# Performance work log

Hardware: AMD Instinct MI355X
Metric: run time of the kernel (lower is better)

## Reference

```python
import jax, jax.numpy as jnp
import numpy as np

B, T, F, H, FC1, NC = 16384, 56, 56, 20, 128, 2


def setup_inputs() -> dict:
    key = jax.random.key(0)
    ks = jax.random.split(key, 12)
    s_in = 1.0 / np.sqrt(H)  # PyTorch GRU init scale
    d = {
        'x': jax.random.normal(ks[0], (B, T, F), jnp.float32),
        'W_ih0': jax.random.uniform(ks[1], (3 * H, F), jnp.float32, -s_in, s_in),
        'W_hh0': jax.random.uniform(ks[2], (3 * H, H), jnp.float32, -s_in, s_in),
        'b_ih0': jax.random.uniform(ks[3], (3 * H,), jnp.float32, -s_in, s_in),
        'b_hh0': jax.random.uniform(ks[4], (3 * H,), jnp.float32, -s_in, s_in),
        'W_ih1': jax.random.uniform(ks[5], (3 * H, H), jnp.float32, -s_in, s_in),
        'W_hh1': jax.random.uniform(ks[6], (3 * H, H), jnp.float32, -s_in, s_in),
        'b_ih1': jax.random.uniform(ks[7], (3 * H,), jnp.float32, -s_in, s_in),
        'b_hh1': jax.random.uniform(ks[8], (3 * H,), jnp.float32, -s_in, s_in),
        'W_fc1': jax.random.uniform(ks[9], (FC1, T * H), jnp.float32, -1 / np.sqrt(T * H), 1 / np.sqrt(T * H)),
        'b_fc1': jnp.zeros((FC1,), jnp.float32),
        'W_fc2': jax.random.uniform(ks[10], (NC, FC1), jnp.float32, -1 / np.sqrt(FC1), 1 / np.sqrt(FC1)),
        'b_fc2': jnp.zeros((NC,), jnp.float32),
    }
    return d


def gru_layer(x, W_ih, W_hh, b_ih, b_hh):
    # x: [B, T, Fin] -> output [B, T, H]; PyTorch gate order: r, z, n
    xproj = jnp.einsum('bti,gi->btg', x, W_ih) + b_ih  # [B, T, 3H]

    def step(h, xp):
        gh = h @ W_hh.T + b_hh
        i_r, i_z, i_n = jnp.split(xp, 3, axis=-1)
        h_r, h_z, h_n = jnp.split(gh, 3, axis=-1)
        r = jax.nn.sigmoid(i_r + h_r)
        z = jax.nn.sigmoid(i_z + h_z)
        n = jnp.tanh(i_n + r * h_n)
        h_new = (1.0 - z) * n + z * h
        return h_new, h_new

    h0 = jnp.zeros((x.shape[0], W_hh.shape[1]), x.dtype)
    _, ys = jax.lax.scan(step, h0, jnp.swapaxes(xproj, 0, 1))  # [T, B, H]
    return jnp.swapaxes(ys, 0, 1)


def reference(x, W_ih0, W_hh0, b_ih0, b_hh0, W_ih1, W_hh1, b_ih1, b_hh1,
              W_fc1, b_fc1, W_fc2, b_fc2):
    h1 = gru_layer(x, W_ih0, W_hh0, b_ih0, b_hh0)   # [B, T, H]
    h2 = gru_layer(h1, W_ih1, W_hh1, b_ih1, b_hh1)  # [B, T, H]
    flat = h2.reshape(h2.shape[0], -1)              # [B, T*H]
    y = flat @ W_fc1.T + b_fc1
    y = y @ W_fc2.T + b_fc2
    return y
```

## Files before the change

### kernel.cpp

```cpp
#include <hip/hip_runtime.h>


#define Bsz  16384
#define Tt   56
#define Ff   56
#define Hh   20
#define Gg   60
#define FC1n 128
#define THn  1120
#define BT   (Bsz * Tt)

#define WS_WEFF 0
#define WS_BEFF 2240
#define WS_WT   2242
#define WS_XP   5632
#define WS_NEED_BYTES ((size_t)(WS_XP + (size_t)BT * Gg) * 4)

typedef __attribute__((address_space(1))) const unsigned char gas_uchar;
typedef __attribute__((address_space(3))) unsigned char las_uchar;
typedef __attribute__((ext_vector_type(2))) float f32x2;

__device__ __forceinline__ float rdlane(float v, int l) {
  return __uint_as_float(__builtin_amdgcn_readlane(__float_as_uint(v), l));
}
__device__ __forceinline__ float bperm(int addr, float v) {
  return __uint_as_float(__builtin_amdgcn_ds_bpermute(addr, __float_as_uint(v)));
}
__device__ __forceinline__ float fast_rcp(float x) { return __builtin_amdgcn_rcpf(x); }
__device__ __forceinline__ float sigmoid_fast(float x) { return fast_rcp(1.0f + __expf(-x)); }
__device__ __forceinline__ float tanh_fast(float x) { return 1.0f - 2.0f * fast_rcp(1.0f + __expf(2.0f * x)); }

__device__ __forceinline__ f32x2 pkfma(f32x2 hs, f32x2 wv, f32x2 c) {
  f32x2 d;
  asm("v_pk_fma_f32 %0, %1, %2, %3" : "=v"(d) : "s"(hs), "v"(wv), "v"(c));
  return d;
}

__device__ __forceinline__ void gru_cell(float xg, float hg, int addrR, int addrZ, float& hm) {
  float sg = sigmoid_fast(xg + hg);
  float rr = bperm(addrR, sg);
  float nn = tanh_fast(fmaf(rr, hg, xg));
  float zz = bperm(addrZ, sg);
  hm = fmaf(zz, hm - nn, nn);
}

__global__ void prep_all(const float* __restrict__ Wfc1, const float* __restrict__ bfc1,
                         const float* __restrict__ Wfc2, const float* __restrict__ bfc2,
                         const float* __restrict__ Wih0, float* __restrict__ ws) {
  int i = blockIdx.x * blockDim.x + threadIdx.x;
  if (i < THn) {
    float s0a = 0.f, s1a = 0.f, s0b = 0.f, s1b = 0.f;
    float s0c = 0.f, s1c = 0.f, s0d = 0.f, s1d = 0.f;
#pragma unroll 4
    for (int j = 0; j < FC1n; j += 4) {
      float wa = Wfc1[(j + 0) * THn + i];
      float wb = Wfc1[(j + 1) * THn + i];
      float wc = Wfc1[(j + 2) * THn + i];
      float wd = Wfc1[(j + 3) * THn + i];
      s0a = fmaf(wa, Wfc2[j + 0], s0a); s1a = fmaf(wa, Wfc2[FC1n + j + 0], s1a);
      s0b = fmaf(wb, Wfc2[j + 1], s0b); s1b = fmaf(wb, Wfc2[FC1n + j + 1], s1b);
      s0c = fmaf(wc, Wfc2[j + 2], s0c); s1c = fmaf(wc, Wfc2[FC1n + j + 2], s1c);
      s0d = fmaf(wd, Wfc2[j + 3], s0d); s1d = fmaf(wd, Wfc2[FC1n + j + 3], s1d);
    }
    ws[WS_WEFF + i * 2 + 0] = (s0a + s0b) + (s0c + s0d);
    ws[WS_WEFF + i * 2 + 1] = (s1a + s1b) + (s1c + s1d);
  } else if (i < THn + 2) {
    int c = i - THn;
    float s = bfc2[c];
    for (int j = 0; j < FC1n; ++j) s = fmaf(bfc1[j], Wfc2[c * FC1n + j], s);
    ws[WS_BEFF + c] = s;
  } else if (i < THn + 2 + 14 * Gg * 4) {
    int j = i - (THn + 2);
    int f4 = j / 240;
    int rem = j % 240;
    int g = rem / 4, c = rem % 4;
    ws[WS_WT + j] = Wih0[g * Ff + f4 * 4 + c];
  }
}

#define PadW 57
__global__ __launch_bounds__(256, 2) void xproj_kernel(
    const float* __restrict__ x, const float* __restrict__ bih0,
    const float* __restrict__ wschunk , float* __restrict__ xp) {
  __shared__ float xs[256 * PadW];
  const int tid = threadIdx.x;
  const size_t blk0 = (size_t)blockIdx.x * 256;

  const float4* xg = (const float4*)(x + blk0 * Ff);
#pragma unroll
  for (int i = 0; i < 14; ++i) {
    int p = i * 256 + tid;
    float4 v = xg[p];
    int r = p / 14, c = p % 14;
    *(float4*)&xs[r * PadW + c * 4] = v;
  }
  __syncthreads();

  float acc[Gg];
#pragma unroll
  for (int g = 0; g < Gg; ++g) acc[g] = bih0[g];

  const float4* wt = (const float4*)wschunk;
#pragma unroll 1
  for (int f4 = 0; f4 < 14; ++f4) {
    float4 xv = *(const float4*)&xs[tid * PadW + f4 * 4];
    const float4* wb = wt + f4 * Gg;
#pragma unroll
    for (int g = 0; g < Gg; ++g) {
      float4 w = wb[g];
      acc[g] = fmaf(xv.x, w.x, fmaf(xv.y, w.y, fmaf(xv.z, w.z, fmaf(xv.w, w.w, acc[g]))));
    }
  }
  float4* out = (float4*)(xp + (blk0 + tid) * Gg);
#pragma unroll
  for (int q = 0; q < 15; ++q)
    out[q] = make_float4(acc[4 * q], acc[4 * q + 1], acc[4 * q + 2], acc[4 * q + 3]);
}

__global__ __launch_bounds__(256, 4) void gru_scan_xp4(
    const float* __restrict__ xp,
    const float* __restrict__ Whh0, const float* __restrict__ bhh0,
    const float* __restrict__ Wih1, const float* __restrict__ bih1,
    const float* __restrict__ Whh1, const float* __restrict__ bhh1,
    const float* __restrict__ ws, float* __restrict__ y) {
  __shared__ float weff[2 * THn + 2];
  for (int idx = threadIdx.x; idx < 2 * THn + 2; idx += 256) weff[idx] = ws[idx];
  __syncthreads();

  const int lane = threadIdx.x & 63;
  const int wv = threadIdx.x >> 6;
  const int b0 = (blockIdx.x * 4 + wv) * 4;
  const int g = (lane < Gg) ? lane : 0;

  f32x2 whh0p[10], wih1p[10], whh1p[10];
#pragma unroll
  for (int i = 0; i < 10; ++i) whh0p[i] = *(const f32x2*)&Whh0[g * Hh + 2 * i];
#pragma unroll
  for (int i = 0; i < 10; ++i) wih1p[i] = *(const f32x2*)&Wih1[g * Hh + 2 * i];
#pragma unroll
  for (int i = 0; i < 10; ++i) whh1p[i] = *(const f32x2*)&Whh1[g * Hh + 2 * i];

  const f32x2 cb0  = {bhh0[g], 0.f};
  const f32x2 cb1i = {bih1[g], 0.f};
  const f32x2 cb1h = {bhh1[g], 0.f};
  const f32x2 zz2  = {0.f, 0.f};

  float hmA[4] = {0.f, 0.f, 0.f, 0.f};
  float hmB[4] = {0.f, 0.f, 0.f, 0.f};
  f32x2 hA2[4][10];
#pragma unroll
  for (int e = 0; e < 4; ++e)
#pragma unroll
    for (int i = 0; i < 10; ++i) hA2[e][i] = zz2;

  float ya[4] = {0.f, 0.f, 0.f, 0.f};
  float yb[4] = {0.f, 0.f, 0.f, 0.f};

  const int addrR = ((lane >= 40) ? (lane - 40) : lane) * 4;
  const int addrZ = ((lane >= 40) ? (lane - 20) : lane) * 4;
  const int jm = (lane >= 40 && lane < Gg) ? lane - 40 : 0;

  const float* xpb = xp + (size_t)b0 * (Tt * Gg);
  int off[4];
  float xc[4], xn[4];
#pragma unroll
  for (int e = 0; e < 4; ++e) { off[e] = e * (Tt * Gg) + g; xc[e] = xpb[off[e]]; }

#pragma unroll 1
  for (int t = 0; t < Tt; ++t) {
    if (t < Tt - 1) {
#pragma unroll
      for (int e = 0; e < 4; ++e) xn[e] = xpb[off[e] + Gg];
    }
#pragma unroll
    for (int e = 0; e < 4; ++e) {
      f32x2 a = pkfma(hA2[e][0], whh0p[0], cb0);
      f32x2 b = pkfma(hA2[e][1], whh0p[1], zz2);
#pragma unroll
      for (int i = 2; i < 10; i += 2) {
        a = pkfma(hA2[e][i], whh0p[i], a);
        b = pkfma(hA2[e][i + 1], whh0p[i + 1], b);
      }
      float hg = (a.x + b.x) + (a.y + b.y);
      gru_cell(xc[e], hg, addrR, addrZ, hmA[e]);
#pragma unroll
      for (int i = 0; i < 10; ++i) {
        f32x2 hp;
        hp.x = rdlane(hmA[e], 40 + 2 * i);
        hp.y = rdlane(hmA[e], 41 + 2 * i);
        hA2[e][i] = hp;
      }
    }
#pragma unroll
    for (int e = 0; e < 4; ++e) {
      f32x2 ai = pkfma(hA2[e][0], wih1p[0], cb1i);
      f32x2 bi = pkfma(hA2[e][1], wih1p[1], zz2);
      f32x2 h0; h0.x = rdlane(hmB[e], 40); h0.y = rdlane(hmB[e], 41);
      f32x2 ah = pkfma(h0, whh1p[0], cb1h);
      f32x2 h1; h1.x = rdlane(hmB[e], 42); h1.y = rdlane(hmB[e], 43);
      f32x2 bh = pkfma(h1, whh1p[1], zz2);
#pragma unroll
      for (int i = 2; i < 10; i += 2) {
        ai = pkfma(hA2[e][i], wih1p[i], ai);
        bi = pkfma(hA2[e][i + 1], wih1p[i + 1], bi);
        f32x2 he; he.x = rdlane(hmB[e], 40 + 2 * i); he.y = rdlane(hmB[e], 41 + 2 * i);
        ah = pkfma(he, whh1p[i], ah);
        f32x2 ho; ho.x = rdlane(hmB[e], 42 + 2 * i); ho.y = rdlane(hmB[e], 43 + 2 * i);
        bh = pkfma(ho, whh1p[i + 1], bh);
      }
      float ig = (ai.x + bi.x) + (ai.y + bi.y);
      float hg = (ah.x + bh.x) + (ah.y + bh.y);
      gru_cell(ig, hg, addrR, addrZ, hmB[e]);
    }
    {
      float2 wv2 = *(const float2*)&weff[(t * Hh + jm) * 2];
#pragma unroll
      for (int e = 0; e < 4; ++e) {
        ya[e] = fmaf(hmB[e], wv2.x, ya[e]);
        yb[e] = fmaf(hmB[e], wv2.y, yb[e]);
      }
    }
#pragma unroll
    for (int e = 0; e < 4; ++e) { xc[e] = xn[e]; off[e] += Gg; }
  }

  const bool active = (lane >= 40 && lane < Gg);
#pragma unroll
  for (int e = 0; e < 4; ++e) {
    if (!active) { ya[e] = 0.f; yb[e] = 0.f; }
  }
#pragma unroll
  for (int off2 = 32; off2 >= 1; off2 >>= 1) {
#pragma unroll
    for (int e = 0; e < 4; ++e) {
      ya[e] += __shfl_xor(ya[e], off2, 64);
      yb[e] += __shfl_xor(yb[e], off2, 64);
    }
  }
  if (lane == 0) {
    float be0 = weff[WS_BEFF], be1 = weff[WS_BEFF + 1];
    float4 o0 = make_float4(ya[0] + be0, yb[0] + be1, ya[1] + be0, yb[1] + be1);
    float4 o1 = make_float4(ya[2] + be0, yb[2] + be1, ya[3] + be0, yb[3] + be1);
    float4* yo = (float4*)(y + (size_t)b0 * 2);
    yo[0] = o0;
    yo[1] = o1;
  }
}

__global__ __launch_bounds__(256) void gru_scan_fb(
    const float* __restrict__ x,
    const float* __restrict__ Wih0, const float* __restrict__ Whh0,
    const float* __restrict__ bih0, const float* __restrict__ bhh0,
    const float* __restrict__ Wih1, const float* __restrict__ Whh1,
    const float* __restrict__ bih1, const float* __restrict__ bhh1,
    const float* __restrict__ ws, float* __restrict__ y) {
  __shared__ float weff[2 * THn];
  __shared__ __align__(16) float xstage[4][2][Ff];
  for (int idx = threadIdx.x; idx < 2 * THn; idx += 256) weff[idx] = ws[idx];
  __syncthreads();

  const int lane = threadIdx.x & 63;
  const int wv = threadIdx.x >> 6;
  const int b = blockIdx.x * 4 + wv;
  const int g = (lane < Gg) ? lane : 0;

  float wih0[Ff], whh0[Hh], wih1[Hh], whh1[Hh];
#pragma unroll
  for (int f = 0; f < Ff; ++f) wih0[f] = Wih0[g * Ff + f];
#pragma unroll
  for (int k = 0; k < Hh; ++k) whh0[k] = Whh0[g * Hh + k];
#pragma unroll
  for (int k = 0; k < Hh; ++k) wih1[k] = Wih1[g * Hh + k];
#pragma unroll
  for (int k = 0; k < Hh; ++k) whh1[k] = Whh1[g * Hh + k];
  const float bi0 = bih0[g], bh0 = bhh0[g], bi1 = bih1[g], bh1 = bhh1[g];

  float sA[Hh], sB[Hh];
#pragma unroll
  for (int k = 0; k < Hh; ++k) { sA[k] = 0.f; sB[k] = 0.f; }
  float hmA = 0.f, hmB = 0.f, y0 = 0.f, y1 = 0.f;

  const float* xrow = x + (size_t)b * (Tt * Ff);
  const int addrR = ((lane >= 40) ? (lane - 40) : lane) * 4;
  const int addrZ = ((lane >= 40) ? (lane - 20) : lane) * 4;
  const int jm = (lane >= 40 && lane < Gg) ? lane - 40 : 0;

  if (lane < 14) {
    __builtin_amdgcn_global_load_lds((gas_uchar*)(xrow + lane * 4),
                                     (las_uchar*)&xstage[wv][0][0], 16, 0, 0);
  }

#pragma unroll 1
  for (int t = 0; t < Tt; ++t) {
    const float* nxt = xrow + ((t < Tt - 1) ? Ff : 0);
    if (lane < 14) {
      __builtin_amdgcn_global_load_lds((gas_uchar*)(nxt + lane * 4),
                                       (las_uchar*)&xstage[wv][(t + 1) & 1][0], 16, 0, 0);
    }
    asm volatile("s_waitcnt vmcnt(1)" ::: "memory");
    const float4* xs = (const float4*)&xstage[wv][t & 1][0];
    {
      float a0 = bi0, a1 = 0.f, a2 = 0.f, a3 = 0.f;
#pragma unroll
      for (int i = 0; i < 14; ++i) {
        float4 xv = xs[i];
        a0 = fmaf(xv.x, wih0[4 * i + 0], a0);
        a1 = fmaf(xv.y, wih0[4 * i + 1], a1);
        a2 = fmaf(xv.z, wih0[4 * i + 2], a2);
        a3 = fmaf(xv.w, wih0[4 * i + 3], a3);
      }
      float ig = (a0 + a1) + (a2 + a3);
      float h0 = bh0, h1v = 0.f;
#pragma unroll
      for (int k = 0; k < Hh; k += 2) {
        h0 = fmaf(sA[k + 0], whh0[k + 0], h0);
        h1v = fmaf(sA[k + 1], whh0[k + 1], h1v);
      }
      float hg = h0 + h1v;
      gru_cell(ig, hg, addrR, addrZ, hmA);
#pragma unroll
      for (int j = 0; j < Hh; ++j) sA[j] = rdlane(hmA, 40 + j);
    }
    {
      float a0 = bi1, a1 = 0.f;
#pragma unroll
      for (int k = 0; k < Hh; k += 2) {
        a0 = fmaf(sA[k + 0], wih1[k + 0], a0);
        a1 = fmaf(sA[k + 1], wih1[k + 1], a1);
      }
      float ig = a0 + a1;
      float h0 = bh1, h1v = 0.f;
#pragma unroll
      for (int k = 0; k < Hh; k += 2) {
        h0 = fmaf(sB[k + 0], whh1[k + 0], h0);
        h1v = fmaf(sB[k + 1], whh1[k + 1], h1v);
      }
      float hg = h0 + h1v;
      gru_cell(ig, hg, addrR, addrZ, hmB);
#pragma unroll
      for (int j = 0; j < Hh; ++j) sB[j] = rdlane(hmB, 40 + j);
    }
    {
      float2 wv2 = *(const float2*)&weff[(t * Hh + jm) * 2];
      y0 = fmaf(hmB, wv2.x, y0);
      y1 = fmaf(hmB, wv2.y, y1);
    }
    xrow += Ff;
  }

  if (!(lane >= 40 && lane < Gg)) { y0 = 0.f; y1 = 0.f; }
#pragma unroll
  for (int off = 32; off >= 1; off >>= 1) {
    y0 += __shfl_xor(y0, off, 64);
    y1 += __shfl_xor(y1, off, 64);
  }
  if (lane == 0) {
    float be0 = ws[WS_BEFF + 0], be1 = ws[WS_BEFF + 1];
    float2 out = make_float2(y0 + be0, y1 + be1);
    *(float2*)(y + (size_t)b * 2) = out;
  }
}

extern "C" void kernel_launch(void* const* d_in, const int* in_sizes, int n_in,
                              void* d_out, int out_size, void* d_ws, size_t ws_size,
                              hipStream_t stream) {
  const float* x    = (const float*)d_in[0];
  const float* Wih0 = (const float*)d_in[1];
  const float* Whh0 = (const float*)d_in[2];
  const float* bih0 = (const float*)d_in[3];
  const float* bhh0 = (const float*)d_in[4];
  const float* Wih1 = (const float*)d_in[5];
  const float* Whh1 = (const float*)d_in[6];
  const float* bih1 = (const float*)d_in[7];
  const float* bhh1 = (const float*)d_in[8];
  const float* Wfc1 = (const float*)d_in[9];
  const float* bfc1 = (const float*)d_in[10];
  const float* Wfc2 = (const float*)d_in[11];
  const float* bfc2 = (const float*)d_in[12];
  float* ws = (float*)d_ws;
  float* y  = (float*)d_out;

  prep_all<<<18, 256, 0, stream>>>(Wfc1, bfc1, Wfc2, bfc2, Wih0, ws);

  if (ws_size >= WS_NEED_BYTES) {
    float* xp = ws + WS_XP;
    xproj_kernel<<<BT / 256, 256, 0, stream>>>(x, bih0, ws + WS_WT, xp);
    gru_scan_xp4<<<Bsz / 16, 256, 0, stream>>>(xp, Whh0, bhh0, Wih1, bih1,
                                               Whh1, bhh1, ws, y);
  } else {
    gru_scan_fb<<<Bsz / 4, 256, 0, stream>>>(x, Wih0, Whh0, bih0, bhh0,
                                             Wih1, Whh1, bih1, bhh1, ws, y);
  }
}
```

Measured before the change: 619.3 us.

## Halve batch rows per wave in GRU scan, stage layer-2 hidden via LDS, pack xproj FMAs

The scan kernel now handles 2 batch rows per wavefront instead of 4 and launches twice as many blocks, which shortens the serial per-step dependency chain per wave and raises parallelism. The layer-2 recurrent hidden state is written to a small per-wave LDS buffer and read back as float4 vectors, replacing 20 readlane scalar broadcasts per row. The input-projection kernel is changed to use packed v_pk_fma_f32 with the x value duplicated and weights loaded as scalar pairs, and the workspace weight transposition is updated to match. The cost is more waves re-reading shared weights, and LDS round-trips on the recurrence that rely on intra-wave ordering with no explicit barrier.

```diff
diff --git a/kernel.cpp b/kernel.cpp
--- a/kernel.cpp
+++ b/kernel.cpp
@@ -30,9 +30,26 @@
 __device__ __forceinline__ float sigmoid_fast(float x) { return fast_rcp(1.0f + __expf(-x)); }
 __device__ __forceinline__ float tanh_fast(float x) { return 1.0f - 2.0f * fast_rcp(1.0f + __expf(2.0f * x)); }
 
-__device__ __forceinline__ f32x2 pkfma(f32x2 hs, f32x2 wv, f32x2 c) {
+__device__ __forceinline__ f32x2 mk2(float a, float b) { f32x2 r; r.x = a; r.y = b; return r; }
+
+__device__ __forceinline__ f32x2 pkfma_s(f32x2 hs, f32x2 wv, f32x2 c) {
   f32x2 d;
   asm("v_pk_fma_f32 %0, %1, %2, %3" : "=v"(d) : "s"(hs), "v"(wv), "v"(c));
+  return d;
+}
+__device__ __forceinline__ f32x2 pkfma_v(f32x2 a, f32x2 b, f32x2 c) {
+  f32x2 d;
+  asm("v_pk_fma_f32 %0, %1, %2, %3" : "=v"(d) : "v"(a), "v"(b), "v"(c));
+  return d;
+}
+__device__ __forceinline__ f32x2 pkfma_w(f32x2 xx, f32x2 w, f32x2 c) {
+  f32x2 d;
+  asm("v_pk_fma_f32 %0, %1, %2, %3" : "=v"(d) : "v"(xx), "s"(w), "v"(c));
+  return d;
+}
+__device__ __forceinline__ f32x2 pkadd(f32x2 a, f32x2 b) {
+  f32x2 d;
+  asm("v_pk_add_f32 %0, %1, %2" : "=v"(d) : "v"(a), "v"(b));
   return d;
 }
 
@@ -69,12 +86,12 @@
     float s = bfc2[c];
     for (int j = 0; j < FC1n; ++j) s = fmaf(bfc1[j], Wfc2[c * FC1n + j], s);
     ws[WS_BEFF + c] = s;
-  } else if (i < THn + 2 + 14 * Gg * 4) {
+  } else if (i < THn + 2 + Ff * Gg) {
     int j = i - (THn + 2);
-    int f4 = j / 240;
-    int rem = j % 240;
-    int g = rem / 4, c = rem % 4;
-    ws[WS_WT + j] = Wih0[g * Ff + f4 * 4 + c];
+    int f = j / 60;
+    int rem = j % 60;
+    int p = rem >> 1, c = rem & 1;
+    ws[WS_WT + j] = Wih0[(2 * p + c) * Ff + f];
   }
 }
 
@@ -96,40 +113,60 @@
   }
   __syncthreads();
 
-  float acc[Gg];
-#pragma unroll
-  for (int g = 0; g < Gg; ++g) acc[g] = bih0[g];
-
-  const float4* wt = (const float4*)wschunk;
+  f32x2 acc2[30];
+  const f32x2* b2 = (const f32x2*)bih0;
+#pragma unroll
+  for (int p = 0; p < 30; ++p) acc2[p] = b2[p];
+
+  const f32x2* wt2 = (const f32x2*)wschunk;
 #pragma unroll 1
   for (int f4 = 0; f4 < 14; ++f4) {
     float4 xv = *(const float4*)&xs[tid * PadW + f4 * 4];
-    const float4* wb = wt + f4 * Gg;
-#pragma unroll
-    for (int g = 0; g < Gg; ++g) {
-      float4 w = wb[g];
-      acc[g] = fmaf(xv.x, w.x, fmaf(xv.y, w.y, fmaf(xv.z, w.z, fmaf(xv.w, w.w, acc[g]))));
+    const f32x2* w0 = wt2 + (size_t)(f4 * 4) * 30;
+    {
+      f32x2 xx = mk2(xv.x, xv.x);
+#pragma unroll
+      for (int p = 0; p < 30; ++p) acc2[p] = pkfma_w(xx, w0[p], acc2[p]);
+    }
+    {
+      f32x2 xx = mk2(xv.y, xv.y);
+      const f32x2* w = w0 + 30;
+#pragma unroll
+      for (int p = 0; p < 30; ++p) acc2[p] = pkfma_w(xx, w[p], acc2[p]);
+    }
+    {
+      f32x2 xx = mk2(xv.z, xv.z);
+      const f32x2* w = w0 + 60;
+#pragma unroll
+      for (int p = 0; p < 30; ++p) acc2[p] = pkfma_w(xx, w[p], acc2[p]);
+    }
+    {
+      f32x2 xx = mk2(xv.w, xv.w);
+      const f32x2* w = w0 + 90;
+#pragma unroll
+      for (int p = 0; p < 30; ++p) acc2[p] = pkfma_w(xx, w[p], acc2[p]);
     }
   }
   float4* out = (float4*)(xp + (blk0 + tid) * Gg);
 #pragma unroll
   for (int q = 0; q < 15; ++q)
-    out[q] = make_float4(acc[4 * q], acc[4 * q + 1], acc[4 * q + 2], acc[4 * q + 3]);
-}
-
-__global__ __launch_bounds__(256, 4) void gru_scan_xp4(
+    out[q] = make_float4(acc2[2 * q].x, acc2[2 * q].y, acc2[2 * q + 1].x, acc2[2 * q + 1].y);
+}
+
+__global__ __launch_bounds__(256, 4) void gru_scan_xp2(
     const float* __restrict__ xp,
     const float* __restrict__ Whh0, const float* __restrict__ bhh0,
     const float* __restrict__ Wih1, const float* __restrict__ bih1,
     const float* __restrict__ Whh1, const float* __restrict__ bhh1,
     const float* __restrict__ ws, float* __restrict__ y) {
   __shared__ float weff[2 * THn + 2];
+  __shared__ __align__(16) float hstage[4][2][64];
   for (int idx = threadIdx.x; idx < 2 * THn + 2; idx += 256) weff[idx] = ws[idx];
   __syncthreads();
 
   const int lane = threadIdx.x & 63;
   const int wv = threadIdx.x >> 6;
-  const int b0 = (blockIdx.x * 4 + wv) * 4;
+  const int b0 = (blockIdx.x * 4 + wv) * 2;
   const int g = (lane < Gg) ? lane : 0;
 
   f32x2 whh0p[10], wih1p[10], whh1p[10];
@@ -140,99 +177,106 @@
 #pragma unroll
   for (int i = 0; i < 10; ++i) whh1p[i] = *(const f32x2*)&Whh1[g * Hh + 2 * i];
 
-  const f32x2 cb0  = {bhh0[g], 0.f};
-  const f32x2 cb1i = {bih1[g], 0.f};
-  const f32x2 cb1h = {bhh1[g], 0.f};
-  const f32x2 zz2  = {0.f, 0.f};
-
-  float hmA[4] = {0.f, 0.f, 0.f, 0.f};
-  float hmB[4] = {0.f, 0.f, 0.f, 0.f};
-  f32x2 hA2[4][10];
-#pragma unroll
-  for (int e = 0; e < 4; ++e)
+  const f32x2 cb0  = mk2(bhh0[g], 0.f);
+  const f32x2 cb1i = mk2(bih1[g], 0.f);
+  const f32x2 cb1h = mk2(bhh1[g], 0.f);
+  const f32x2 zz2  = mk2(0.f, 0.f);
+
+  float hmA[2] = {0.f, 0.f};
+  float hmB[2] = {0.f, 0.f};
+  f32x2 hA2[2][10];
+#pragma unroll
+  for (int e = 0; e < 2; ++e)
 #pragma unroll
     for (int i = 0; i < 10; ++i) hA2[e][i] = zz2;
 
-  float ya[4] = {0.f, 0.f, 0.f, 0.f};
-  float yb[4] = {0.f, 0.f, 0.f, 0.f};
+  hstage[wv][0][lane] = 0.f;
+  hstage[wv][1][lane] = 0.f;
+
+  float ya[2] = {0.f, 0.f};
+  float yb[2] = {0.f, 0.f};
 
   const int addrR = ((lane >= 40) ? (lane - 40) : lane) * 4;
   const int addrZ = ((lane >= 40) ? (lane - 20) : lane) * 4;
   const int jm = (lane >= 40 && lane < Gg) ? lane - 40 : 0;
 
   const float* xpb = xp + (size_t)b0 * (Tt * Gg);
-  int off[4];
-  float xc[4], xn[4];
-#pragma unroll
-  for (int e = 0; e < 4; ++e) { off[e] = e * (Tt * Gg) + g; xc[e] = xpb[off[e]]; }
+  int off[2];
+  float xc[2], xn[2];
+#pragma unroll
+  for (int e = 0; e < 2; ++e) { off[e] = e * (Tt * Gg) + g; xc[e] = xpb[off[e]]; }
 
 #pragma unroll 1
   for (int t = 0; t < Tt; ++t) {
     if (t < Tt - 1) {
 #pragma unroll
-      for (int e = 0; e < 4; ++e) xn[e] = xpb[off[e] + Gg];
-    }
-#pragma unroll
-    for (int e = 0; e < 4; ++e) {
-      f32x2 a = pkfma(hA2[e][0], whh0p[0], cb0);
-      f32x2 b = pkfma(hA2[e][1], whh0p[1], zz2);
+      for (int e = 0; e < 2; ++e) xn[e] = xpb[off[e] + Gg];
+    }
+#pragma unroll
+    for (int e = 0; e < 2; ++e) {
+      f32x2 a = pkfma_s(hA2[e][0], whh0p[0], cb0);
+      f32x2 b = pkfma_s(hA2[e][1], whh0p[1], zz2);
 #pragma unroll
       for (int i = 2; i < 10; i += 2) {
-        a = pkfma(hA2[e][i], whh0p[i], a);
-        b = pkfma(hA2[e][i + 1], whh0p[i + 1], b);
-      }
-      float hg = (a.x + b.x) + (a.y + b.y);
+        a = pkfma_s(hA2[e][i], whh0p[i], a);
+        b = pkfma_s(hA2[e][i + 1], whh0p[i + 1], b);
+      }
+      f32x2 s = pkadd(a, b);
+      float hg = s.x + s.y;
       gru_cell(xc[e], hg, addrR, addrZ, hmA[e]);
 #pragma unroll
-      for (int i = 0; i < 10; ++i) {
-        f32x2 hp;
-        hp.x = rdlane(hmA[e], 40 + 2 * i);
-        hp.y = rdlane(hmA[e], 41 + 2 * i);
-        hA2[e][i] = hp;
-      }
-    }
-#pragma unroll
-    for (int e = 0; e < 4; ++e) {
-      f32x2 ai = pkfma(hA2[e][0], wih1p[0], cb1i);
-      f32x2 bi = pkfma(hA2[e][1], wih1p[1], zz2);
-      f32x2 h0; h0.x = rdlane(hmB[e], 40); h0.y = rdlane(hmB[e], 41);
-      f32x2 ah = pkfma(h0, whh1p[0], cb1h);
-      f32x2 h1; h1.x = rdlane(hmB[e], 42); h1.y = rdlane(hmB[e], 43);
-      f32x2 bh = pkfma(h1, whh1p[1], zz2);
+      for (int i = 0; i < 10; ++i)
+        hA2[e][i] = mk2(rdlane(hmA[e], 40 + 2 * i), rdlane(hmA[e], 41 + 2 * i));
+    }
+#pragma unroll
+    for (int e = 0; e < 2; ++e) {
+      f32x2 ai = pkfma_s(hA2[e][0], wih1p[0], cb1i);
+      f32x2 bi = pkfma_s(hA2[e][1], wih1p[1], zz2);
 #pragma unroll
       for (int i = 2; i < 10; i += 2) {
-        ai = pkfma(hA2[e][i], wih1p[i], ai);
-        bi = pkfma(hA2[e][i + 1], wih1p[i + 1], bi);
-        f32x2 he; he.x = rdlane(hmB[e], 40 + 2 * i); he.y = rdlane(hmB[e], 41 + 2 * i);
-        ah = pkfma(he, whh1p[i], ah);
-        f32x2 ho; ho.x = rdlane(hmB[e], 42 + 2 * i); ho.y = rdlane(hmB[e], 43 + 2 * i);
-        bh = pkfma(ho, whh1p[i + 1], bh);
-      }
-      float ig = (ai.x + bi.x) + (ai.y + bi.y);
-      float hg = (ah.x + bh.x) + (ah.y + bh.y);
+        ai = pkfma_s(hA2[e][i], wih1p[i], ai);
+        bi = pkfma_s(hA2[e][i + 1], wih1p[i + 1], bi);
+      }
+      const float4* hb = (const float4*)&hstage[wv][e][40];
+      float4 q0 = hb[0], q1 = hb[1], q2 = hb[2], q3 = hb[3], q4 = hb[4];
+      f32x2 ah = pkfma_v(mk2(q0.x, q0.y), whh1p[0], cb1h);
+      f32x2 bh = pkfma_v(mk2(q0.z, q0.w), whh1p[1], zz2);
+      ah = pkfma_v(mk2(q1.x, q1.y), whh1p[2], ah);
+      bh = pkfma_v(mk2(q1.z, q1.w), whh1p[3], bh);
+      ah = pkfma_v(mk2(q2.x, q2.y), whh1p[4], ah);
+      bh = pkfma_v(mk2(q2.z, q2.w), whh1p[5], bh);
+      ah = pkfma_v(mk2(q3.x, q3.y), whh1p[6], ah);
+      bh = pkfma_v(mk2(q3.z, q3.w), whh1p[7], bh);
+      ah = pkfma_v(mk2(q4.x, q4.y), whh1p[8], ah);
+      bh = pkfma_v(mk2(q4.z, q4.w), whh1p[9], bh);
+      f32x2 si = pkadd(ai, bi);
+      float ig = si.x + si.y;
+      f32x2 sh = pkadd(ah, bh);
+      float hg = sh.x + sh.y;
       gru_cell(ig, hg, addrR, addrZ, hmB[e]);
+      hstage[wv][e][lane] = hmB[e];
     }
     {
       float2 wv2 = *(const float2*)&weff[(t * Hh + jm) * 2];
 #pragma unroll
-      for (int e = 0; e < 4; ++e) {
+      for (int e = 0; e < 2; ++e) {
         ya[e] = fmaf(hmB[e], wv2.x, ya[e]);
         yb[e] = fmaf(hmB[e], wv2.y, yb[e]);
       }
     }
 #pragma unroll
-    for (int e = 0; e < 4; ++e) { xc[e] = xn[e]; off[e] += Gg; }
+    for (int e = 0; e < 2; ++e) { xc[e] = xn[e]; off[e] += Gg; }
   }
 
   const bool active = (lane >= 40 && lane < Gg);
 #pragma unroll
-  for (int e = 0; e < 4; ++e) {
+  for (int e = 0; e < 2; ++e) {
     if (!active) { ya[e] = 0.f; yb[e] = 0.f; }
   }
 #pragma unroll
   for (int off2 = 32; off2 >= 1; off2 >>= 1) {
 #pragma unroll
-    for (int e = 0; e < 4; ++e) {
+    for (int e = 0; e < 2; ++e) {
       ya[e] += __shfl_xor(ya[e], off2, 64);
       yb[e] += __shfl_xor(yb[e], off2, 64);
     }
@@ -240,10 +284,7 @@
   if (lane == 0) {
     float be0 = weff[WS_BEFF], be1 = weff[WS_BEFF + 1];
     float4 o0 = make_float4(ya[0] + be0, yb[0] + be1, ya[1] + be0, yb[1] + be1);
-    float4 o1 = make_float4(ya[2] + be0, yb[2] + be1, ya[3] + be0, yb[3] + be1);
-    float4* yo = (float4*)(y + (size_t)b0 * 2);
-    yo[0] = o0;
-    yo[1] = o1;
+    *(float4*)(y + (size_t)b0 * 2) = o0;
   }
 }
 
@@ -385,8 +426,8 @@
   if (ws_size >= WS_NEED_BYTES) {
     float* xp = ws + WS_XP;
     xproj_kernel<<<BT / 256, 256, 0, stream>>>(x, bih0, ws + WS_WT, xp);
-    gru_scan_xp4<<<Bsz / 16, 256, 0, stream>>>(xp, Whh0, bhh0, Wih1, bih1,
-                                               Whh1, bhh1, ws, y);
+    gru_scan_xp2<<<Bsz / 8, 256, 0, stream>>>(xp, Whh0, bhh0, Wih1, bih1,
+                                              Whh1, bhh1, ws, y);
   } else {
     gru_scan_fb<<<Bsz / 4, 256, 0, stream>>>(x, Wih0, Whh0, bih0, bhh0,
                                              Wih1, Whh1, bih1, bhh1, ws, y);
```

Result: faster. 566.6 us (-8.5%).
